# Performance work log

Measured on AMD Instinct MI355X. Metric: run time of the kernel, lower is better.

Reference implementation:

```python
import jax, jax.numpy as jnp
import numpy as np

B, T, E, H, P = 512, 512, 64, 128, 96


def setup_inputs() -> dict:
    key = jax.random.key(0)
    ks = jax.random.split(key, 12)
    s = 1.0 / np.sqrt(H)  # torch GRU/Linear uniform init scale
    u = lambda k, shape: jax.random.uniform(k, shape, jnp.float32, -s, s)
    return {
        "x": jax.random.normal(ks[0], (B, T, E), jnp.float32),
        "W_ih0": u(ks[1], (3 * H, E)),
        "W_hh0": u(ks[2], (3 * H, H)),
        "b_ih0": u(ks[3], (3 * H,)),
        "b_hh0": u(ks[4], (3 * H,)),
        "W_ih1": u(ks[5], (3 * H, H)),
        "W_hh1": u(ks[6], (3 * H, H)),
        "b_ih1": u(ks[7], (3 * H,)),
        "b_hh1": u(ks[8], (3 * H,)),
        "W_head": u(ks[9], (P, H)),
        "b_head": u(ks[10], (P,)),
    }


def _gru_layer(x, W_ih, W_hh, b_ih, b_hh):
    # x: [B, T, F]; PyTorch gate order: r, z, n
    Bn, Tn, _ = x.shape
    Hn = W_hh.shape[1]
    # precompute input-side gates for all timesteps: [B, T, 3H]
    xg = jnp.einsum('btf,gf->btg', x, W_ih) + b_ih

    def step(h, xg_t):
        hg = h @ W_hh.T + b_hh                      # [B, 3H]
        xr, xz, xn = jnp.split(xg_t, 3, axis=-1)
        hr, hz, hn = jnp.split(hg, 3, axis=-1)
        r = jax.nn.sigmoid(xr + hr)
        z = jax.nn.sigmoid(xz + hz)
        n = jnp.tanh(xn + r * hn)
        h_new = (1.0 - z) * n + z * h
        return h_new, h_new

    h0 = jnp.zeros((Bn, Hn), x.dtype)
    _, ys = jax.lax.scan(step, h0, jnp.swapaxes(xg, 0, 1))  # ys: [T, B, H]
    return jnp.swapaxes(ys, 0, 1)                            # [B, T, H]


def reference(x, W_ih0, W_hh0, b_ih0, b_hh0, W_ih1, W_hh1, b_ih1, b_hh1, W_head, b_head):
    h1 = _gru_layer(x, W_ih0, W_hh0, b_ih0, b_hh0)
    h2 = _gru_layer(h1, W_ih1, W_hh1, b_ih1, b_hh1)
    last = h2[:, -1, :]                   # [B, H]
    return last @ W_head.T + b_head       # [B, pred_len]
```

## Files before the change

### kernel.cpp

```cpp
#include <hip/hip_runtime.h>


#define B_SZ 512
#define T_SZ 512
#define E_SZ 64
#define H_SZ 128
#define P_SZ 96
#define NB   16
#define NGRP (B_SZ / NB)
#define SC_SIG  (-1.44269504f)
#define SC_TANH (-2.88539008f)

typedef _Float16 half8 __attribute__((ext_vector_type(8)));
typedef float    f32x4 __attribute__((ext_vector_type(4)));

__device__ __forceinline__ float exp2_(float x) {
#if __has_builtin(__builtin_amdgcn_exp2f)
    return __builtin_amdgcn_exp2f(x);
#else
    return exp2f(x);
#endif
}
__device__ __forceinline__ float rcp_(float x) {
#if __has_builtin(__builtin_amdgcn_rcpf)
    return __builtin_amdgcn_rcpf(x);
#else
    return 1.0f / x;
#endif
}

__device__ __forceinline__ int swz256(int row, int byte) {
    return row * 256 + (byte ^ ((row & 7) << 4));
}

__device__ __forceinline__ void load_bfrag(const float* __restrict__ W, int ldk,
                                           int n0, int kt, int ln, float scale,
                                           half8* hi) {
    int n = n0 + (ln & 15);
    int k = kt * 32 + (ln >> 4) * 8;
    const float* p = W + (size_t)n * ldk + k;
    float4 a = *(const float4*)p;
    float4 b = *(const float4*)(p + 4);
    float v[8] = {a.x, a.y, a.z, a.w, b.x, b.y, b.z, b.w};
    half8 h;
    #pragma unroll
    for (int j = 0; j < 8; ++j)
        h[j] = (_Float16)(v[j] * scale);
    *hi = h;
}

#define LOADX(Sx, tt)                                                              \
    if ((tt) < T_SZ) {                                                             \
        _Pragma("unroll") for (int kt = 0; kt < KFX; ++kt)                         \
            Sx[kt] = *(const half8*)(xlane + (size_t)(tt) * ROWB + kt * 64);       \
    }

#define GRU_STEP(Sx, tcur, tnext)                                                  \
    {                                                                              \
        const char* hb = hs[(tcur) & 1];                                           \
        half8 ah[4];                                                               \
        _Pragma("unroll") for (int kt = 0; kt < 4; ++kt)                           \
            ah[kt] = *(const half8*)(hb + swz256(colg, kt * 64 + rgrp * 16));      \
        f32x4 ax0 = {bs0, bs0, bs0, bs0};                                          \
        f32x4 ax1 = {bs1, bs1, bs1, bs1};                                          \
        f32x4 ax2 = {bi2s, bi2s, bi2s, bi2s};                                      \
        f32x4 ah2 = {bh2s, bh2s, bh2s, bh2s};                                      \
        f32x4 ah0 = {0.f, 0.f, 0.f, 0.f};                                          \
        f32x4 ah1 = ah0;                                                           \
        _Pragma("unroll") for (int kt = 0; kt < KFX; ++kt) {                       \
            ax0 = __builtin_amdgcn_mfma_f32_16x16x32_f16(Sx[kt], bx[0][kt], ax0, 0, 0, 0); \
            ax1 = __builtin_amdgcn_mfma_f32_16x16x32_f16(Sx[kt], bx[1][kt], ax1, 0, 0, 0); \
            ax2 = __builtin_amdgcn_mfma_f32_16x16x32_f16(Sx[kt], bx[2][kt], ax2, 0, 0, 0); \
        }                                                                          \
        __builtin_amdgcn_s_setprio(1);                                             \
        _Pragma("unroll") for (int kt = 0; kt < 4; ++kt) {                         \
            ah0 = __builtin_amdgcn_mfma_f32_16x16x32_f16(ah[kt], bhh[0][kt], ah0, 0, 0, 0); \
            ah1 = __builtin_amdgcn_mfma_f32_16x16x32_f16(ah[kt], bhh[1][kt], ah1, 0, 0, 0); \
            ah2 = __builtin_amdgcn_mfma_f32_16x16x32_f16(ah[kt], bhh[2][kt], ah2, 0, 0, 0); \
        }                                                                          \
        LOADX(Sx, tnext)                                                           \
        float hn_[4];                                                              \
        _Pragma("unroll") for (int j = 0; j < 4; ++j) {                            \
            float rr = rcp_(1.f + exp2_(ax0[j] + ah0[j]));                         \
            float zz = rcp_(1.f + exp2_(ax1[j] + ah1[j]));                         \
            float v  = ax2[j] + rr * ah2[j];                                       \
            float nn = fmaf(2.f, rcp_(1.f + exp2_(v)), -1.f);                      \
            hn_[j] = nn + zz * (hreg[j] - nn);                                     \
            hreg[j] = hn_[j];                                                      \
        }                                                                          \
        __builtin_amdgcn_s_setprio(0);                                             \
        char* hw = hs[((tcur) + 1) & 1];                                           \
        _Pragma("unroll") for (int j = 0; j < 4; ++j) {                            \
            int bb = rgrp * 4 + j;                                                 \
            *(_Float16*)(hw + swz256(bb, cw * 2)) = (_Float16)hn_[j];              \
            if constexpr (OUT_ALL) {                                               \
                ((_Float16*)hout)[((size_t)(b0 + bb) * T_SZ + (tcur)) * H_SZ + cw] \
                    = (_Float16)hn_[j];                                            \
            } else {                                                               \
                if ((tcur) == T_SZ - 1)                                            \
                    ((float*)hout)[(size_t)(b0 + bb) * H_SZ + cw] = hn_[j];        \
            }                                                                      \
        }                                                                          \
           \
        asm volatile("s_waitcnt lgkmcnt(0)" ::: "memory");                         \
        __builtin_amdgcn_s_barrier();                                              \
        __builtin_amdgcn_sched_barrier(0);                                         \
    }

template<int K_IN, bool OUT_ALL, int ROLE>
__device__ __forceinline__ void gru_body(const _Float16* __restrict__ xin,
                                         const float* __restrict__ W_ih,
                                         const float* __restrict__ W_hh,
                                         const float* __restrict__ b_ih,
                                         const float* __restrict__ b_hh,
                                         void* __restrict__ hout,
                                         int* __restrict__ prog,
                                         int grp, char (*hs)[4096])
{
    constexpr int KFX  = K_IN / 32;
    constexpr int ROWB = K_IN * 2;

    const int tid  = threadIdx.x;
    const int ln   = tid & 63;
    const int wv   = tid >> 6;
    const int colg = ln & 15;
    const int rgrp = ln >> 4;
    const int b0   = grp * NB;
    const int cw   = wv * 16 + colg;

    half8 bx[3][KFX];
    half8 bhh[3][4];
    const float gsc[3] = {SC_SIG, SC_SIG, SC_TANH};
    #pragma unroll
    for (int g = 0; g < 3; ++g) {
        int n0 = g * 128 + wv * 16;
        #pragma unroll
        for (int kt = 0; kt < KFX; ++kt)
            load_bfrag(W_ih, K_IN, n0, kt, ln, gsc[g], &bx[g][kt]);
        #pragma unroll
        for (int kt = 0; kt < 4; ++kt)
            load_bfrag(W_hh, H_SZ, n0, kt, ln, gsc[g], &bhh[g][kt]);
    }
    const float bs0  = SC_SIG  * (b_ih[cw] + b_hh[cw]);
    const float bs1  = SC_SIG  * (b_ih[128 + cw] + b_hh[128 + cw]);
    const float bi2s = SC_TANH * b_ih[256 + cw];
    const float bh2s = SC_TANH * b_hh[256 + cw];

    if (tid < 256) *(float4*)(hs[0] + tid * 16) = make_float4(0.f, 0.f, 0.f, 0.f);
    float hreg[4] = {0.f, 0.f, 0.f, 0.f};

    const char* xlane = (const char*)xin
        + (size_t)(b0 + colg) * T_SZ * ROWB
        + rgrp * 16;

    int avail = 0;
    if (ROLE == 1) {
        while (avail < 4) {
            avail = __hip_atomic_load(prog, __ATOMIC_ACQUIRE, __HIP_MEMORY_SCOPE_AGENT);
            if (avail < 4) __builtin_amdgcn_s_sleep(8);
        }
    }

    half8 Ax[KFX], Bx2[KFX];
    LOADX(Ax, 0)
    LOADX(Bx2, 1)
    __syncthreads();

    for (int t = 0; t < T_SZ; t += 2) {
        if (ROLE == 1 && avail < T_SZ) {
            const int need = (t + 4 < T_SZ) ? t + 4 : T_SZ;
            while (avail < need) {
                avail = __hip_atomic_load(prog, __ATOMIC_ACQUIRE, __HIP_MEMORY_SCOPE_AGENT);
                if (avail < need) __builtin_amdgcn_s_sleep(8);
            }
        }
        GRU_STEP(Ax,  t,     t + 2)
        GRU_STEP(Bx2, t + 1, t + 3)
        if (ROLE == 0 && (t & 7) == 6) {
            asm volatile("s_waitcnt vmcnt(0)" ::: "memory");
            __builtin_amdgcn_s_barrier();
            if (tid == 0)
                __hip_atomic_store(prog, t + 2, __ATOMIC_RELEASE, __HIP_MEMORY_SCOPE_AGENT);
        }
    }
}

__global__ __launch_bounds__(512)
void gru_fused(const _Float16* __restrict__ xh,
               _Float16* __restrict__ h1,
               float* __restrict__ h2,
               const float* __restrict__ W_ih0, const float* __restrict__ W_hh0,
               const float* __restrict__ b_ih0, const float* __restrict__ b_hh0,
               const float* __restrict__ W_ih1, const float* __restrict__ W_hh1,
               const float* __restrict__ b_ih1, const float* __restrict__ b_hh1,
               int* __restrict__ prog)
{
    __shared__ __align__(16) char hs[2][4096];
    const int role = blockIdx.x >> 5;
    const int grp  = blockIdx.x & 31;
    if (role == 0)
        gru_body<E_SZ, true, 0>(xh, W_ih0, W_hh0, b_ih0, b_hh0, h1, prog + grp, grp, hs);
    else
        gru_body<H_SZ, false, 1>(h1, W_ih1, W_hh1, b_ih1, b_hh1, h2, prog + grp, grp, hs);
}

__global__ __launch_bounds__(256)
void cvt_f32_f16(const float* __restrict__ in, _Float16* __restrict__ out, int n8)
{
    int i = blockIdx.x * 256 + threadIdx.x;
    if (i >= n8) return;
    const float4* p = (const float4*)in + (size_t)i * 2;
    float4 a = p[0];
    float4 b = p[1];
    half8 h;
    h[0] = (_Float16)a.x; h[1] = (_Float16)a.y; h[2] = (_Float16)a.z; h[3] = (_Float16)a.w;
    h[4] = (_Float16)b.x; h[5] = (_Float16)b.y; h[6] = (_Float16)b.z; h[7] = (_Float16)b.w;
    ((half8*)out)[i] = h;
}

__global__ __launch_bounds__(256)
void head_kernel(const float* __restrict__ h2,
                 const float* __restrict__ W,
                 const float* __restrict__ bias,
                 float* __restrict__ out)
{
    int idx = blockIdx.x * 256 + threadIdx.x;
    if (idx >= B_SZ * P_SZ) return;
    int b = idx / P_SZ;
    int p = idx % P_SZ;
    const float* hv = h2 + b * H_SZ;
    const float* wv = W + p * H_SZ;
    float a0 = 0.f, a1 = 0.f, a2 = 0.f, a3 = 0.f;
    #pragma unroll
    for (int i = 0; i < H_SZ; i += 4) {
        float4 h4 = *(const float4*)(hv + i);
        float4 w4 = *(const float4*)(wv + i);
        a0 += h4.x * w4.x;
        a1 += h4.y * w4.y;
        a2 += h4.z * w4.z;
        a3 += h4.w * w4.w;
    }
    out[idx] = (a0 + a1) + (a2 + a3) + bias[p];
}

extern "C" void kernel_launch(void* const* d_in, const int* in_sizes, int n_in,
                              void* d_out, int out_size, void* d_ws, size_t ws_size,
                              hipStream_t stream)
{
    const float* x      = (const float*)d_in[0];
    const float* W_ih0  = (const float*)d_in[1];
    const float* W_hh0  = (const float*)d_in[2];
    const float* b_ih0  = (const float*)d_in[3];
    const float* b_hh0  = (const float*)d_in[4];
    const float* W_ih1  = (const float*)d_in[5];
    const float* W_hh1  = (const float*)d_in[6];
    const float* b_ih1  = (const float*)d_in[7];
    const float* b_hh1  = (const float*)d_in[8];
    const float* W_head = (const float*)d_in[9];
    const float* b_head = (const float*)d_in[10];
    float* out = (float*)d_out;

    char* ws = (char*)d_ws;
    _Float16* h1  = (_Float16*)ws;
    _Float16* xh  = (_Float16*)(ws + (64u << 20));
    float*    h2  = (float*)   (ws + (96u << 20));
    int*      prg = (int*)     (ws + (96u << 20) + (256u << 10));

    hipMemsetAsync(prg, 0, NGRP * sizeof(int), stream);
    cvt_f32_f16<<<(B_SZ * T_SZ * E_SZ / 8 + 255) / 256, 256, 0, stream>>>(x, xh, B_SZ * T_SZ * E_SZ / 8);
    gru_fused<<<2 * NGRP, 512, 0, stream>>>(xh, h1, h2,
                                            W_ih0, W_hh0, b_ih0, b_hh0,
                                            W_ih1, W_hh1, b_ih1, b_hh1, prg);
    head_kernel<<<(B_SZ * P_SZ + 255) / 256, 256, 0, stream>>>(h2, W_head, b_head, out);
}
```

Baseline: 514.1 us.

## Software-pipeline input-gate MFMAs one step ahead and merge progress barrier

Input-side gate products for step t+1 are now computed during step t, after the recurrent MFMAs, and accumulated directly into the recurrent r/z accumulators. This takes the input projection off the serial dependency chain, so each step only waits on the hidden-state MFMAs before the activations. The separate progress-publish barrier is folded into the per-step barrier, and the consumer spin-wait sleep is shortened. In exchange, register pressure rises from the extra live accumulators.

```diff
diff --git a/kernel.cpp b/kernel.cpp
--- a/kernel.cpp
+++ b/kernel.cpp
@@ -55,35 +55,33 @@
             Sx[kt] = *(const half8*)(xlane + (size_t)(tt) * ROWB + kt * 64);       \
     }
 
-#define GRU_STEP(Sx, tcur, tnext)                                                  \
+#define GRU_STEP(Xd, Xl, P_R, P_Z, P_N, Q_R, Q_Z, Q_N, tcur)                       \
     {                                                                              \
         const char* hb = hs[(tcur) & 1];                                           \
         half8 ah[4];                                                               \
         _Pragma("unroll") for (int kt = 0; kt < 4; ++kt)                           \
             ah[kt] = *(const half8*)(hb + swz256(colg, kt * 64 + rgrp * 16));      \
-        f32x4 ax0 = {bs0, bs0, bs0, bs0};                                          \
-        f32x4 ax1 = {bs1, bs1, bs1, bs1};                                          \
-        f32x4 ax2 = {bi2s, bi2s, bi2s, bi2s};                                      \
-        f32x4 ah2 = {bh2s, bh2s, bh2s, bh2s};                                      \
-        f32x4 ah0 = {0.f, 0.f, 0.f, 0.f};                                          \
-        f32x4 ah1 = ah0;                                                           \
-        _Pragma("unroll") for (int kt = 0; kt < KFX; ++kt) {                       \
-            ax0 = __builtin_amdgcn_mfma_f32_16x16x32_f16(Sx[kt], bx[0][kt], ax0, 0, 0, 0); \
-            ax1 = __builtin_amdgcn_mfma_f32_16x16x32_f16(Sx[kt], bx[1][kt], ax1, 0, 0, 0); \
-            ax2 = __builtin_amdgcn_mfma_f32_16x16x32_f16(Sx[kt], bx[2][kt], ax2, 0, 0, 0); \
-        }                                                                          \
+        f32x4 cNH = {bh2s, bh2s, bh2s, bh2s};                                      \
         __builtin_amdgcn_s_setprio(1);                                             \
         _Pragma("unroll") for (int kt = 0; kt < 4; ++kt) {                         \
-            ah0 = __builtin_amdgcn_mfma_f32_16x16x32_f16(ah[kt], bhh[0][kt], ah0, 0, 0, 0); \
-            ah1 = __builtin_amdgcn_mfma_f32_16x16x32_f16(ah[kt], bhh[1][kt], ah1, 0, 0, 0); \
-            ah2 = __builtin_amdgcn_mfma_f32_16x16x32_f16(ah[kt], bhh[2][kt], ah2, 0, 0, 0); \
-        }                                                                          \
-        LOADX(Sx, tnext)                                                           \
+            P_R = __builtin_amdgcn_mfma_f32_16x16x32_f16(ah[kt], bhh[0][kt], P_R, 0, 0, 0); \
+            P_Z = __builtin_amdgcn_mfma_f32_16x16x32_f16(ah[kt], bhh[1][kt], P_Z, 0, 0, 0); \
+            cNH = __builtin_amdgcn_mfma_f32_16x16x32_f16(ah[kt], bhh[2][kt], cNH, 0, 0, 0); \
+        }                                                                          \
+        Q_R = (f32x4){bs0, bs0, bs0, bs0};                                         \
+        Q_Z = (f32x4){bs1, bs1, bs1, bs1};                                         \
+        Q_N = (f32x4){bi2s, bi2s, bi2s, bi2s};                                     \
+        _Pragma("unroll") for (int kt = 0; kt < KFX; ++kt) {                       \
+            Q_R = __builtin_amdgcn_mfma_f32_16x16x32_f16(Xl[kt], bx[0][kt], Q_R, 0, 0, 0); \
+            Q_Z = __builtin_amdgcn_mfma_f32_16x16x32_f16(Xl[kt], bx[1][kt], Q_Z, 0, 0, 0); \
+            Q_N = __builtin_amdgcn_mfma_f32_16x16x32_f16(Xl[kt], bx[2][kt], Q_N, 0, 0, 0); \
+        }                                                                          \
+        LOADX(Xd, (tcur) + 2)                                                      \
         float hn_[4];                                                              \
         _Pragma("unroll") for (int j = 0; j < 4; ++j) {                            \
-            float rr = rcp_(1.f + exp2_(ax0[j] + ah0[j]));                         \
-            float zz = rcp_(1.f + exp2_(ax1[j] + ah1[j]));                         \
-            float v  = ax2[j] + rr * ah2[j];                                       \
+            float rr = rcp_(1.f + exp2_(P_R[j]));                                  \
+            float zz = rcp_(1.f + exp2_(P_Z[j]));                                  \
+            float v  = P_N[j] + rr * cNH[j];                                       \
             float nn = fmaf(2.f, rcp_(1.f + exp2_(v)), -1.f);                      \
             hn_[j] = nn + zz * (hreg[j] - nn);                                     \
             hreg[j] = hn_[j];                                                      \
@@ -101,9 +99,17 @@
                     ((float*)hout)[(size_t)(b0 + bb) * H_SZ + cw] = hn_[j];        \
             }                                                                      \
         }                                                                          \
-           \
-        asm volatile("s_waitcnt lgkmcnt(0)" ::: "memory");                         \
-        __builtin_amdgcn_s_barrier();                                              \
+        if (ROLE == 0 && (((tcur) & 7) == 7)) {                                    \
+             \
+            asm volatile("s_waitcnt vmcnt(0) lgkmcnt(0)" ::: "memory");            \
+            __builtin_amdgcn_s_barrier();                                          \
+            if (tid == 0)                                                          \
+                __hip_atomic_store(prog, (tcur) + 1, __ATOMIC_RELEASE,             \
+                                   __HIP_MEMORY_SCOPE_AGENT);                      \
+        } else {                                                                   \
+            asm volatile("s_waitcnt lgkmcnt(0)" ::: "memory");                     \
+            __builtin_amdgcn_s_barrier();                                          \
+        }                                                                          \
         __builtin_amdgcn_sched_barrier(0);                                         \
     }
 
@@ -157,13 +163,24 @@
     if (ROLE == 1) {
         while (avail < 4) {
             avail = __hip_atomic_load(prog, __ATOMIC_ACQUIRE, __HIP_MEMORY_SCOPE_AGENT);
-            if (avail < 4) __builtin_amdgcn_s_sleep(8);
+            if (avail < 4) __builtin_amdgcn_s_sleep(2);
         }
     }
 
-    half8 Ax[KFX], Bx2[KFX];
-    LOADX(Ax, 0)
-    LOADX(Bx2, 1)
+    half8 Xa[KFX], Xb[KFX];
+    LOADX(Xa, 0)
+    LOADX(Xb, 1)
+
+    f32x4 P0R, P0Z, P0N, P1R, P1Z, P1N;
+    P0R = (f32x4){bs0, bs0, bs0, bs0};
+    P0Z = (f32x4){bs1, bs1, bs1, bs1};
+    P0N = (f32x4){bi2s, bi2s, bi2s, bi2s};
+    #pragma unroll
+    for (int kt = 0; kt < KFX; ++kt) {
+        P0R = __builtin_amdgcn_mfma_f32_16x16x32_f16(Xa[kt], bx[0][kt], P0R, 0, 0, 0);
+        P0Z = __builtin_amdgcn_mfma_f32_16x16x32_f16(Xa[kt], bx[1][kt], P0Z, 0, 0, 0);
+        P0N = __builtin_amdgcn_mfma_f32_16x16x32_f16(Xa[kt], bx[2][kt], P0N, 0, 0, 0);
+    }
     __syncthreads();
 
     for (int t = 0; t < T_SZ; t += 2) {
@@ -171,17 +188,11 @@
             const int need = (t + 4 < T_SZ) ? t + 4 : T_SZ;
             while (avail < need) {
                 avail = __hip_atomic_load(prog, __ATOMIC_ACQUIRE, __HIP_MEMORY_SCOPE_AGENT);
-                if (avail < need) __builtin_amdgcn_s_sleep(8);
+                if (avail < need) __builtin_amdgcn_s_sleep(2);
             }
         }
-        GRU_STEP(Ax,  t,     t + 2)
-        GRU_STEP(Bx2, t + 1, t + 3)
-        if (ROLE == 0 && (t & 7) == 6) {
-            asm volatile("s_waitcnt vmcnt(0)" ::: "memory");
-            __builtin_amdgcn_s_barrier();
-            if (tid == 0)
-                __hip_atomic_store(prog, t + 2, __ATOMIC_RELEASE, __HIP_MEMORY_SCOPE_AGENT);
-        }
+        GRU_STEP(Xa, Xb, P0R, P0Z, P0N, P1R, P1Z, P1N, t)
+        GRU_STEP(Xb, Xa, P1R, P1Z, P1N, P0R, P0Z, P0N, t + 1)
     }
 }
 
```

Measured after the change: 523.9 us. About the same (+1.9%).

## Fuse head projection into GRU kernel and merge gate accumulators

Applied to the files above, without the earlier changes.

Removes the separate head kernel. The layer-2 blocks compute the final linear projection with MFMA from the last hidden state in shared memory and write the output directly, which also drops the h2 workspace. In the recurrence step, the hidden-side r/z MFMAs now accumulate into the same registers as the input-side ones, which saves adds and registers. The cost is a longer serial MFMA dependency chain within each step.

```diff
diff --git a/kernel.cpp b/kernel.cpp
--- a/kernel.cpp
+++ b/kernel.cpp
@@ -64,9 +64,7 @@
         f32x4 ax0 = {bs0, bs0, bs0, bs0};                                          \
         f32x4 ax1 = {bs1, bs1, bs1, bs1};                                          \
         f32x4 ax2 = {bi2s, bi2s, bi2s, bi2s};                                      \
-        f32x4 ah2 = {bh2s, bh2s, bh2s, bh2s};                                      \
-        f32x4 ah0 = {0.f, 0.f, 0.f, 0.f};                                          \
-        f32x4 ah1 = ah0;                                                           \
+        f32x4 cNH = {bh2s, bh2s, bh2s, bh2s};                                      \
         _Pragma("unroll") for (int kt = 0; kt < KFX; ++kt) {                       \
             ax0 = __builtin_amdgcn_mfma_f32_16x16x32_f16(Sx[kt], bx[0][kt], ax0, 0, 0, 0); \
             ax1 = __builtin_amdgcn_mfma_f32_16x16x32_f16(Sx[kt], bx[1][kt], ax1, 0, 0, 0); \
@@ -74,16 +72,16 @@
         }                                                                          \
         __builtin_amdgcn_s_setprio(1);                                             \
         _Pragma("unroll") for (int kt = 0; kt < 4; ++kt) {                         \
-            ah0 = __builtin_amdgcn_mfma_f32_16x16x32_f16(ah[kt], bhh[0][kt], ah0, 0, 0, 0); \
-            ah1 = __builtin_amdgcn_mfma_f32_16x16x32_f16(ah[kt], bhh[1][kt], ah1, 0, 0, 0); \
-            ah2 = __builtin_amdgcn_mfma_f32_16x16x32_f16(ah[kt], bhh[2][kt], ah2, 0, 0, 0); \
+            ax0 = __builtin_amdgcn_mfma_f32_16x16x32_f16(ah[kt], bhh[0][kt], ax0, 0, 0, 0); \
+            ax1 = __builtin_amdgcn_mfma_f32_16x16x32_f16(ah[kt], bhh[1][kt], ax1, 0, 0, 0); \
+            cNH = __builtin_amdgcn_mfma_f32_16x16x32_f16(ah[kt], bhh[2][kt], cNH, 0, 0, 0); \
         }                                                                          \
         LOADX(Sx, tnext)                                                           \
         float hn_[4];                                                              \
         _Pragma("unroll") for (int j = 0; j < 4; ++j) {                            \
-            float rr = rcp_(1.f + exp2_(ax0[j] + ah0[j]));                         \
-            float zz = rcp_(1.f + exp2_(ax1[j] + ah1[j]));                         \
-            float v  = ax2[j] + rr * ah2[j];                                       \
+            float rr = rcp_(1.f + exp2_(ax0[j]));                                  \
+            float zz = rcp_(1.f + exp2_(ax1[j]));                                  \
+            float v  = ax2[j] + rr * cNH[j];                                       \
             float nn = fmaf(2.f, rcp_(1.f + exp2_(v)), -1.f);                      \
             hn_[j] = nn + zz * (hreg[j] - nn);                                     \
             hreg[j] = hn_[j];                                                      \
@@ -96,9 +94,6 @@
             if constexpr (OUT_ALL) {                                               \
                 ((_Float16*)hout)[((size_t)(b0 + bb) * T_SZ + (tcur)) * H_SZ + cw] \
                     = (_Float16)hn_[j];                                            \
-            } else {                                                               \
-                if ((tcur) == T_SZ - 1)                                            \
-                    ((float*)hout)[(size_t)(b0 + bb) * H_SZ + cw] = hn_[j];        \
             }                                                                      \
         }                                                                          \
            \
@@ -114,6 +109,9 @@
                                          const float* __restrict__ b_ih,
                                          const float* __restrict__ b_hh,
                                          void* __restrict__ hout,
+                                         const float* __restrict__ W_head,
+                                         const float* __restrict__ b_head,
+                                         float* __restrict__ out,
                                          int* __restrict__ prog,
                                          int grp, char (*hs)[4096])
 {
@@ -145,6 +143,15 @@
     const float bs1  = SC_SIG  * (b_ih[128 + cw] + b_hh[128 + cw]);
     const float bi2s = SC_TANH * b_ih[256 + cw];
     const float bh2s = SC_TANH * b_hh[256 + cw];
+
+    half8 bph[4];
+    float bhd = 0.f;
+    if (ROLE == 1 && wv < 6) {
+        #pragma unroll
+        for (int kt = 0; kt < 4; ++kt)
+            load_bfrag(W_head, H_SZ, wv * 16, kt, ln, 1.0f, &bph[kt]);
+        bhd = b_head[cw];
+    }
 
     if (tid < 256) *(float4*)(hs[0] + tid * 16) = make_float4(0.f, 0.f, 0.f, 0.f);
     float hreg[4] = {0.f, 0.f, 0.f, 0.f};
@@ -183,25 +190,42 @@
                 __hip_atomic_store(prog, t + 2, __ATOMIC_RELEASE, __HIP_MEMORY_SCOPE_AGENT);
         }
     }
+
+    if (ROLE == 1 && wv < 6) {
+        half8 ahf[4];
+        #pragma unroll
+        for (int kt = 0; kt < 4; ++kt)
+            ahf[kt] = *(const half8*)(hs[0] + swz256(colg, kt * 64 + rgrp * 16));
+        f32x4 acc = {bhd, bhd, bhd, bhd};
+        #pragma unroll
+        for (int kt = 0; kt < 4; ++kt)
+            acc = __builtin_amdgcn_mfma_f32_16x16x32_f16(ahf[kt], bph[kt], acc, 0, 0, 0);
+        #pragma unroll
+        for (int j = 0; j < 4; ++j)
+            out[(size_t)(b0 + rgrp * 4 + j) * P_SZ + cw] = acc[j];
+    }
 }
 
 __global__ __launch_bounds__(512)
 void gru_fused(const _Float16* __restrict__ xh,
                _Float16* __restrict__ h1,
-               float* __restrict__ h2,
                const float* __restrict__ W_ih0, const float* __restrict__ W_hh0,
                const float* __restrict__ b_ih0, const float* __restrict__ b_hh0,
                const float* __restrict__ W_ih1, const float* __restrict__ W_hh1,
                const float* __restrict__ b_ih1, const float* __restrict__ b_hh1,
+               const float* __restrict__ W_head, const float* __restrict__ b_head,
+               float* __restrict__ out,
                int* __restrict__ prog)
 {
     __shared__ __align__(16) char hs[2][4096];
     const int role = blockIdx.x >> 5;
     const int grp  = blockIdx.x & 31;
     if (role == 0)
-        gru_body<E_SZ, true, 0>(xh, W_ih0, W_hh0, b_ih0, b_hh0, h1, prog + grp, grp, hs);
+        gru_body<E_SZ, true, 0>(xh, W_ih0, W_hh0, b_ih0, b_hh0, h1,
+                                W_head, b_head, out, prog + grp, grp, hs);
     else
-        gru_body<H_SZ, false, 1>(h1, W_ih1, W_hh1, b_ih1, b_hh1, h2, prog + grp, grp, hs);
+        gru_body<H_SZ, false, 1>(h1, W_ih1, W_hh1, b_ih1, b_hh1, nullptr,
+                                 W_head, b_head, out, prog + grp, grp, hs);
 }
 
 __global__ __launch_bounds__(256)
@@ -216,31 +240,6 @@
     h[0] = (_Float16)a.x; h[1] = (_Float16)a.y; h[2] = (_Float16)a.z; h[3] = (_Float16)a.w;
     h[4] = (_Float16)b.x; h[5] = (_Float16)b.y; h[6] = (_Float16)b.z; h[7] = (_Float16)b.w;
     ((half8*)out)[i] = h;
-}
-
-__global__ __launch_bounds__(256)
-void head_kernel(const float* __restrict__ h2,
-                 const float* __restrict__ W,
-                 const float* __restrict__ bias,
-                 float* __restrict__ out)
-{
-    int idx = blockIdx.x * 256 + threadIdx.x;
-    if (idx >= B_SZ * P_SZ) return;
-    int b = idx / P_SZ;
-    int p = idx % P_SZ;
-    const float* hv = h2 + b * H_SZ;
-    const float* wv = W + p * H_SZ;
-    float a0 = 0.f, a1 = 0.f, a2 = 0.f, a3 = 0.f;
-    #pragma unroll
-    for (int i = 0; i < H_SZ; i += 4) {
-        float4 h4 = *(const float4*)(hv + i);
-        float4 w4 = *(const float4*)(wv + i);
-        a0 += h4.x * w4.x;
-        a1 += h4.y * w4.y;
-        a2 += h4.z * w4.z;
-        a3 += h4.w * w4.w;
-    }
-    out[idx] = (a0 + a1) + (a2 + a3) + bias[p];
 }
 
 extern "C" void kernel_launch(void* const* d_in, const int* in_sizes, int n_in,
@@ -263,13 +262,12 @@
     char* ws = (char*)d_ws;
     _Float16* h1  = (_Float16*)ws;
     _Float16* xh  = (_Float16*)(ws + (64u << 20));
-    float*    h2  = (float*)   (ws + (96u << 20));
-    int*      prg = (int*)     (ws + (96u << 20) + (256u << 10));
+    int*      prg = (int*)     (ws + (96u << 20));
 
     hipMemsetAsync(prg, 0, NGRP * sizeof(int), stream);
     cvt_f32_f16<<<(B_SZ * T_SZ * E_SZ / 8 + 255) / 256, 256, 0, stream>>>(x, xh, B_SZ * T_SZ * E_SZ / 8);
-    gru_fused<<<2 * NGRP, 512, 0, stream>>>(xh, h1, h2,
+    gru_fused<<<2 * NGRP, 512, 0, stream>>>(xh, h1,
                                             W_ih0, W_hh0, b_ih0, b_hh0,
-                                            W_ih1, W_hh1, b_ih1, b_hh1, prg);
-    head_kernel<<<(B_SZ * P_SZ + 255) / 256, 256, 0, stream>>>(h2, W_head, b_head, out);
-}
+                                            W_ih1, W_hh1, b_ih1, b_hh1,
+                                            W_head, b_head, out, prg);
+}
```

Result: no change. 512.4 us (-0.3%).
